# Optimization experiments

Hardware: AMD Instinct MI355X
Metric: run time of the kernel (lower is better)

## Reference

```python
import jax, jax.numpy as jnp
import numpy as np

N, E, B, IN, H = 20000, 50000, 1024, 32, 64

def setup_inputs() -> dict:
    key = jax.random.key(0)
    ks = jax.random.split(key, 32)
    d = {}
    d["x"] = jax.random.normal(ks[0], (N, IN), jnp.float32)
    d["edge_index"] = jax.random.randint(ks[1], (2, E), 0, N)
    d["edge_attr"] = jax.random.uniform(ks[2], (E, 6), dtype=jnp.float32)
    d["batch"] = jnp.sort(jax.random.randint(ks[3], (N,), 0, B))
    d["t"] = jax.random.uniform(ks[4], (B, 1), dtype=jnp.float32)
    d["p"] = jax.random.uniform(ks[5], (B, 1), dtype=jnp.float32)
    d["num_graphs"] = B
    def lin(k, fan_in, shape):
        return jax.random.normal(k, shape, jnp.float32) * (1.0 / np.sqrt(fan_in))
    # lin0: IN -> H
    d["W0"] = lin(ks[6], IN, (IN, H)); d["b0"] = jnp.zeros((H,), jnp.float32)
    # edge MLP: 6 -> 64 -> H*H
    d["We1"] = lin(ks[7], 6, (6, 64)); d["be1"] = jnp.zeros((64,), jnp.float32)
    d["We2"] = lin(ks[8], 64, (64, H * H)); d["be2"] = jnp.zeros((H * H,), jnp.float32)
    # NNConv root weight + bias
    d["Wroot"] = lin(ks[9], H, (H, H)); d["bconv"] = jnp.zeros((H,), jnp.float32)
    # GRU (input H, hidden H), torch layout [3H, *] gate order r,z,n
    d["gru_wih"] = lin(ks[10], H, (3 * H, H)); d["gru_whh"] = lin(ks[11], H, (3 * H, H))
    d["gru_bih"] = jnp.zeros((3 * H,), jnp.float32); d["gru_bhh"] = jnp.zeros((3 * H,), jnp.float32)
    # Set2Set LSTM (input 2H, hidden H), torch layout [4H, *] gate order i,f,g,o
    d["l_wih"] = lin(ks[12], 2 * H, (4 * H, 2 * H)); d["l_whh"] = lin(ks[13], H, (4 * H, H))
    d["l_bih"] = jnp.zeros((4 * H,), jnp.float32); d["l_bhh"] = jnp.zeros((4 * H,), jnp.float32)
    # readout MLP
    d["W1"] = lin(ks[14], 2 * H + 2, (2 * H + 2, H)); d["b1"] = jnp.zeros((H,), jnp.float32)
    d["W2"] = lin(ks[15], H, (H, 64)); d["b2"] = jnp.zeros((64,), jnp.float32)
    d["W3"] = lin(ks[16], 64, (64, 1)); d["b3"] = jnp.zeros((1,), jnp.float32)
    return d


def reference(x, edge_attr, t, p, W0, b0, We1, be1, We2, be2, Wroot, bconv,
              gru_wih, gru_whh, gru_bih, gru_bhh, l_wih, l_whh, l_bih, l_bhh,
              W1, b1, W2, b2, W3, b3, edge_index, batch, num_graphs):
    n_nodes = x.shape[0]
    hdim = W0.shape[1]
    src, dst = edge_index[0], edge_index[1]

    out = jax.nn.relu(x @ W0 + b0)            # [N,H]
    h = out

    # edge MLP -> per-edge weight matrices [E,H,H] (edge_attr is loop-invariant)
    ew = (jax.nn.relu(edge_attr @ We1 + be1) @ We2 + be2).reshape(-1, hdim, hdim)

    for _ in range(4):
        # NNConv: gather source features, per-edge matmul, scatter-add to targets
        msg = jnp.einsum('eh,eho->eo', out[src], ew)                 # [E,H]
        agg = jax.ops.segment_sum(msg, dst, num_segments=n_nodes)    # [N,H]
        m = jax.nn.relu(agg + out @ Wroot + bconv)
        # GRU step (single timestep)
        gi = m @ gru_wih.T + gru_bih
        gh = h @ gru_whh.T + gru_bhh
        ir, iz, inn = jnp.split(gi, 3, axis=-1)
        hr, hz, hn = jnp.split(gh, 3, axis=-1)
        r = jax.nn.sigmoid(ir + hr)
        z = jax.nn.sigmoid(iz + hz)
        nn_ = jnp.tanh(inn + r * hn)
        h = (1.0 - z) * nn_ + z * h
        out = h

    # Set2Set pooling, 3 processing steps
    qh = jnp.zeros((num_graphs, hdim), x.dtype)
    qc = jnp.zeros((num_graphs, hdim), x.dtype)
    q_star = jnp.zeros((num_graphs, 2 * hdim), x.dtype)
    for _ in range(3):
        g = q_star @ l_wih.T + l_bih + qh @ l_whh.T + l_bhh
        gi_, gf_, gg_, go_ = jnp.split(g, 4, axis=-1)
        qc = jax.nn.sigmoid(gf_) * qc + jax.nn.sigmoid(gi_) * jnp.tanh(gg_)
        qh = jax.nn.sigmoid(go_) * jnp.tanh(qc)
        q = qh                                                        # [B,H]
        e = jnp.sum(out * q[batch], axis=-1, keepdims=True)          # [N,1]
        emax = jax.ops.segment_max(e, batch, num_segments=num_graphs)
        a = jnp.exp(e - emax[batch])
        asum = jax.ops.segment_sum(a, batch, num_segments=num_graphs)
        a = a / asum[batch]                                           # segment softmax
        r_ = jax.ops.segment_sum(a * out, batch, num_segments=num_graphs)
        q_star = jnp.concatenate([q, r_], axis=-1)

    feat = jnp.concatenate([q_star, t, p], axis=-1)                   # [B,2H+2]
    y = jax.nn.relu(feat @ W1 + b1)
    y = jax.nn.relu(y @ W2 + b2)
    y = y @ W3 + b3
    return y.reshape(-1)
```

## Files before the change

kernel.cpp:

```cpp
#include <hip/hip_runtime.h>
#include <math.h>

#define N_NODES 20000
#define N_EDGES 50000
#define NB      1024
#define IND     32
#define HDIM    64

typedef __attribute__((ext_vector_type(8))) short bf16x8;
typedef __attribute__((ext_vector_type(4))) float f32x4;

static inline size_t align_up(size_t x, size_t a) { return (x + a - 1) & ~(a - 1); }

__device__ __forceinline__ float sigmoidf_(float x) {
    return 1.0f / (1.0f + __expf(-x));
}
__device__ __forceinline__ float tanhf_(float x) {
    float xc = fminf(fmaxf(x, -15.0f), 15.0f);
    float e = __expf(2.0f * xc);
    return (e - 1.0f) / (e + 1.0f);
}
__device__ __forceinline__ unsigned pk2(float p0, float p1) {
    unsigned u0 = __float_as_uint(p0) + 0x8000u;
    unsigned u1 = __float_as_uint(p1) + 0x8000u;
    return __builtin_amdgcn_perm(u1, u0, 0x07060302u);
}
__device__ __forceinline__ unsigned bf1(float v) {
    return (__float_as_uint(v) + 0x8000u) >> 16;
}

__global__ void k_prep(const float* __restrict__ We2, const float* __restrict__ be2,
                       short* __restrict__ We2b,
                       const float* __restrict__ Wroot, const float* __restrict__ gwhh,
                       const float* __restrict__ gwih,
                       short* __restrict__ WB1h, short* __restrict__ WB1l,
                       short* __restrict__ WB2h, short* __restrict__ WB2l,
                       const float* __restrict__ lwih, const float* __restrict__ lwhh,
                       float* __restrict__ lwihT, float* __restrict__ lwhhT,
                       const int* __restrict__ batch, int* __restrict__ offs,
                       const float* __restrict__ x, const float* __restrict__ W0,
                       const float* __restrict__ b0, float* __restrict__ hbuf,
                       const float* __restrict__ ea, const float* __restrict__ We1,
                       const float* __restrict__ be1, float* __restrict__ re,
                       const int* __restrict__ ei, int* __restrict__ deg) {
    int bid = blockIdx.x, tid = threadIdx.x;
    if (bid < 1040) {
        int idx = bid * 256 + tid;
        int s = idx >> 12;
        int col = idx & 4095;
        int k = col >> 6, o = col & 63;
        float val = (s < 64) ? We2[k * 4096 + s * 64 + o] : be2[k * 64 + o];
        int dst = s * 4096 + (((o >> 4) * 128 + (k >> 5) * 64 + ((k >> 3) & 3) * 16 + (o & 15)) << 3) + (k & 7);
        We2b[dst] = (short)bf1(val);
    } else if (bid < 1152) {
        int idx = (bid - 1040) * 256 + tid;
        if (idx < 28672) {
            bool b1 = idx < 16384;
            int li = b1 ? idx : idx - 16384;
            int j = li & 7, lane = (li >> 3) & 63, c = (li >> 9) & 1, otile = li >> 10;
            int k = c * 32 + (lane >> 4) * 8 + j;
            int o = otile * 16 + (lane & 15);
            float val;
            if (b1) val = (o < 64) ? Wroot[k * 64 + o] : gwhh[(o - 64) * 64 + k];
            else    val = gwih[o * 64 + k];
            unsigned hs = bf1(val);
            float lo = val - __uint_as_float(hs << 16);
            unsigned ls = bf1(lo);
            if (b1) { WB1h[li] = (short)hs; WB1l[li] = (short)ls; }
            else    { WB2h[li] = (short)hs; WB2l[li] = (short)ls; }
        }
    } else if (bid < 1280) {
        int idx = (bid - 1152) * 256 + tid;
        int i = idx >> 8, j = idx & 255;
        lwihT[idx] = lwih[j * 128 + i];
    } else if (bid < 1344) {
        int idx = (bid - 1280) * 256 + tid;
        int i = idx >> 8, j = idx & 255;
        lwhhT[idx] = lwhh[j * 64 + i];
    } else if (bid < 1349) {
        int i = (bid - 1344) * 256 + tid;
        if (i <= NB) {
            int lo = 0, hi = N_NODES;
            while (lo < hi) { int mid = (lo + hi) >> 1; if (batch[mid] < i) lo = mid + 1; else hi = mid; }
            offs[i] = lo;
        }
    } else if (bid < 6349) {
        int w = tid >> 6, j = tid & 63;
        int n = (bid - 1349) * 4 + w;
        float acc = b0[j];
        const float* xr = x + n * IND;
#pragma unroll
        for (int i = 0; i < IND; ++i) acc = fmaf(xr[i], W0[i * 64 + j], acc);
        hbuf[n * 64 + j] = fmaxf(acc, 0.0f);
    } else if (bid < 18849) {
        int w = tid >> 6, j = tid & 63;
        int e = (bid - 6349) * 4 + w;
        if (e < N_EDGES) {
            float acc = be1[j];
            const float* er = ea + e * 6;
#pragma unroll
            for (int i = 0; i < 6; ++i) acc = fmaf(er[i], We1[i * 64 + j], acc);
            re[e * 64 + j] = fmaxf(acc, 0.0f);
        }
    } else {
        int e = (bid - 18849) * 256 + tid;
        if (e < N_EDGES) atomicAdd(&deg[ei[N_EDGES + e]], 1);
    }
}

__global__ void k_scan(const int* __restrict__ deg, int* __restrict__ rowptr, int* __restrict__ cursor) {
    __shared__ int s_w[16];
    int t = threadIdx.x;
    int base = t * 20;
    int v[20]; int s = 0;
#pragma unroll
    for (int i = 0; i < 20; ++i) {
        int idx = base + i;
        v[i] = (idx < N_NODES) ? deg[idx] : 0;
        s += v[i];
    }
    int lane = t & 63, w = t >> 6;
    int inc = s;
#pragma unroll
    for (int off = 1; off < 64; off <<= 1) {
        int o = __shfl_up(inc, off);
        if (lane >= off) inc += o;
    }
    if (lane == 63) s_w[w] = inc;
    __syncthreads();
    if (w == 0 && lane < 16) {
        int x = s_w[lane];
        int xs = x;
#pragma unroll
        for (int off = 1; off < 16; off <<= 1) {
            int o = __shfl_up(xs, off);
            if (lane >= off) xs += o;
        }
        s_w[lane] = xs - x;
    }
    __syncthreads();
    int run = s_w[w] + (inc - s);
#pragma unroll
    for (int i = 0; i < 20; ++i) {
        int idx = base + i;
        if (idx < N_NODES) { rowptr[idx] = run; cursor[idx] = run; }
        else if (idx == N_NODES) rowptr[idx] = run;
        run += v[i];
    }
}

__global__ void k_fill(const int* __restrict__ ei, int* __restrict__ cursor, int* __restrict__ perm) {
    int e = blockIdx.x * 256 + threadIdx.x;
    if (e < N_EDGES) {
        int pos = atomicAdd(&cursor[ei[N_EDGES + e]], 1);
        perm[pos] = e;
    }
}

#define MSG_STEP_COMPUTE(BB0, BB1, PP)                                                              \
    _Pragma("unroll")                                                                               \
    for (int m = 0; m < 4; ++m) {                                                                   \
        f32x4 tt = __builtin_amdgcn_mfma_f32_16x16x32_bf16(BB0.v, a_re[m][0].v, zero4, 0, 0, 0);    \
        tt = __builtin_amdgcn_mfma_f32_16x16x32_bf16(BB1.v, a_re[m][1].v, tt, 0, 0, 0);             \
        macc[m][0] = fmaf(vsc[PP][m], tt[0], macc[m][0]);                                           \
        macc[m][1] = fmaf(vsc[PP][m], tt[1], macc[m][1]);                                           \
        macc[m][2] = fmaf(vsc[PP][m], tt[2], macc[m][2]);                                           \
        macc[m][3] = fmaf(vsc[PP][m], tt[3], macc[m][3]);                                           \
    }

__launch_bounds__(256, 4)
__global__ void k_msg_mfma(const float* __restrict__ hbuf, const float* __restrict__ reb,
                           const short* __restrict__ We2b, const int* __restrict__ ei,
                           float* __restrict__ msg) {
    __shared__ union {
        float v[64][64];
        float out[64][68];
    } s_u;
    int tid = threadIdx.x;
    int eb = blockIdx.x * 64;
    int lane = tid & 63;
    int w = tid >> 6;
    int l15 = lane & 15, lhi = lane >> 4;

    {
        int se = tid >> 2;
        int sh = tid & 3;
        int ge = eb + se;
        const float* rowp = (ge < N_EDGES) ? (hbuf + (size_t)ei[ge] * 64) : (const float*)0;
#pragma unroll
        for (int rr4 = 0; rr4 < 4; ++rr4) {
            int hb = rr4 * 16 + sh * 4;
            float4 vv = rowp ? *(const float4*)(rowp + hb) : make_float4(0.f, 0.f, 0.f, 0.f);
            s_u.v[hb + 0][se] = vv.x; s_u.v[hb + 1][se] = vv.y;
            s_u.v[hb + 2][se] = vv.z; s_u.v[hb + 3][se] = vv.w;
        }
    }

    union U { int4 i4; bf16x8 v; };
    U a_re[4][2];
#pragma unroll
    for (int m = 0; m < 4; ++m) {
        int ge = eb + m * 16 + l15;
        if (ge < N_EDGES) {
            const float* rp = reb + (size_t)ge * 64 + lhi * 8;
            float4 x0 = *(const float4*)(rp);
            float4 x1 = *(const float4*)(rp + 4);
            float4 y0 = *(const float4*)(rp + 32);
            float4 y1 = *(const float4*)(rp + 36);
            a_re[m][0].i4 = make_int4(pk2(x0.x, x0.y), pk2(x0.z, x0.w), pk2(x1.x, x1.y), pk2(x1.z, x1.w));
            a_re[m][1].i4 = make_int4(pk2(y0.x, y0.y), pk2(y0.z, y0.w), pk2(y1.x, y1.y), pk2(y1.z, y1.w));
        } else {
            a_re[m][0].i4 = make_int4(0, 0, 0, 0);
            a_re[m][1].i4 = make_int4(0, 0, 0, 0);
        }
    }

    const int4* bp0 = (const int4*)We2b + (w * 128 + lane);
    const int4* bp1 = bp0 + 64;
    int4 Sc0[4], Sc1[4];
#pragma unroll
    for (int j = 0; j < 4; ++j) {
        Sc0[j] = bp0[j * 512];
        Sc1[j] = bp1[j * 512];
    }

    __syncthreads();

    const f32x4 zero4 = {0.f, 0.f, 0.f, 0.f};
    f32x4 macc[4];
#pragma unroll
    for (int m = 0; m < 4; ++m) macc[m] = zero4;

    float vsc[2][4];
#pragma unroll
    for (int m = 0; m < 4; ++m) vsc[0][m] = s_u.v[0][m * 16 + l15];

    for (int g = 0; g < 16; ++g) {
#pragma unroll
        for (int j = 0; j < 4; ++j) {
            const int p = j & 1, q = p ^ 1;
            int s = g * 4 + j;
            int snext = (s < 63) ? (s + 1) : 63;
#pragma unroll
            for (int m = 0; m < 4; ++m) vsc[q][m] = s_u.v[snext][m * 16 + l15];
            U bb0, bb1; bb0.i4 = Sc0[j]; bb1.i4 = Sc1[j];
            MSG_STEP_COMPUTE(bb0, bb1, p)
            int sload = (s + 4 <= 64) ? (s + 4) : 64;
            Sc0[j] = bp0[sload * 512];
            Sc1[j] = bp1[sload * 512];
        }
    }

    {
        U bb0, bb1; bb0.i4 = Sc0[0]; bb1.i4 = Sc1[0];
#pragma unroll
        for (int m = 0; m < 4; ++m) {
            int e = m * 16 + l15;
            U a0, a1;
            a0.i4 = make_int4(
                pk2(s_u.v[lhi * 8 + 0][e], s_u.v[lhi * 8 + 1][e]),
                pk2(s_u.v[lhi * 8 + 2][e], s_u.v[lhi * 8 + 3][e]),
                pk2(s_u.v[lhi * 8 + 4][e], s_u.v[lhi * 8 + 5][e]),
                pk2(s_u.v[lhi * 8 + 6][e], s_u.v[lhi * 8 + 7][e]));
            a1.i4 = make_int4(
                pk2(s_u.v[32 + lhi * 8 + 0][e], s_u.v[32 + lhi * 8 + 1][e]),
                pk2(s_u.v[32 + lhi * 8 + 2][e], s_u.v[32 + lhi * 8 + 3][e]),
                pk2(s_u.v[32 + lhi * 8 + 4][e], s_u.v[32 + lhi * 8 + 5][e]),
                pk2(s_u.v[32 + lhi * 8 + 6][e], s_u.v[32 + lhi * 8 + 7][e]));
            macc[m] = __builtin_amdgcn_mfma_f32_16x16x32_bf16(bb0.v, a0.v, macc[m], 0, 0, 0);
            macc[m] = __builtin_amdgcn_mfma_f32_16x16x32_bf16(bb1.v, a1.v, macc[m], 0, 0, 0);
        }
    }

    __syncthreads();
#pragma unroll
    for (int m = 0; m < 4; ++m) {
        *(float4*)&s_u.out[m * 16 + l15][w * 16 + lhi * 4] =
            make_float4(macc[m][0], macc[m][1], macc[m][2], macc[m][3]);
    }
    __syncthreads();
    {
        int er = tid >> 2, qc = tid & 3;
        int ge = eb + er;
        if (ge < N_EDGES) {
#pragma unroll
            for (int i = 0; i < 4; ++i)
                *(float4*)&msg[(size_t)ge * 64 + qc * 16 + i * 4] =
                    *(const float4*)&s_u.out[er][qc * 16 + i * 4];
        }
    }
}

__launch_bounds__(256, 4)
__global__ void k_node_update(float* __restrict__ hbuf, const float* __restrict__ msg,
                              const int* __restrict__ rowptr, const int* __restrict__ perm,
                              const short* __restrict__ WB1h, const short* __restrict__ WB1l,
                              const short* __restrict__ WB2h, const short* __restrict__ WB2l,
                              const float* __restrict__ bconv, const float* __restrict__ bih,
                              const float* __restrict__ bhh) {
    __shared__ short s_hh[32][72];
    __shared__ short s_hl[32][72];
    __shared__ short s_mh[32][72];
    __shared__ short s_ml[32][72];
    __shared__ float s_agg[32][68];
    int tid = threadIdx.x;
    int nbase = blockIdx.x * 32;
    int lane = tid & 63, w = tid >> 6;
    int l15 = lane & 15, lhi = lane >> 4;

    {
        int nt = tid >> 3, q = tid & 7;
        int n = nbase + nt;
#pragma unroll
        for (int c4 = 0; c4 < 2; ++c4) {
            int col = q * 8 + c4 * 4;
            float4 v = *(const float4*)&hbuf[(size_t)n * 64 + col];
            unsigned h01 = pk2(v.x, v.y), h23 = pk2(v.z, v.w);
            float f0 = __uint_as_float(h01 << 16);
            float f1 = __uint_as_float(h01 & 0xffff0000u);
            float f2 = __uint_as_float(h23 << 16);
            float f3 = __uint_as_float(h23 & 0xffff0000u);
            unsigned l01 = pk2(v.x - f0, v.y - f1), l23 = pk2(v.z - f2, v.w - f3);
            *(unsigned*)&s_hh[nt][col]     = h01;
            *(unsigned*)&s_hh[nt][col + 2] = h23;
            *(unsigned*)&s_hl[nt][col]     = l01;
            *(unsigned*)&s_hl[nt][col + 2] = l23;
        }
        float4 aggv[2];
#pragma unroll
        for (int c4 = 0; c4 < 2; ++c4)
            aggv[c4] = *(const float4*)&bconv[q * 8 + c4 * 4];
        int rs = rowptr[n], rend = rowptr[n + 1];
        for (int qq = rs; qq < rend; ++qq) {
            const float* mrow = msg + (size_t)perm[qq] * 64 + q * 8;
#pragma unroll
            for (int c4 = 0; c4 < 2; ++c4) {
                float4 mv = *(const float4*)&mrow[c4 * 4];
                aggv[c4].x += mv.x; aggv[c4].y += mv.y;
                aggv[c4].z += mv.z; aggv[c4].w += mv.w;
            }
        }
#pragma unroll
        for (int c4 = 0; c4 < 2; ++c4)
            *(float4*)&s_agg[nt][q * 8 + c4 * 4] = aggv[c4];
    }
    __syncthreads();

    union U { int4 i4; bf16x8 v; };
    U ah[2][2], al[2][2];
#pragma unroll
    for (int m = 0; m < 2; ++m)
#pragma unroll
        for (int c = 0; c < 2; ++c) {
            ah[m][c].i4 = *(const int4*)&s_hh[m * 16 + l15][c * 32 + lhi * 8];
            al[m][c].i4 = *(const int4*)&s_hl[m * 16 + l15][c * 32 + lhi * 8];
        }

    const int4* B1h = (const int4*)WB1h;
    const int4* B1l = (const int4*)WB1l;
    const int4* B2h = (const int4*)WB2h;
    const int4* B2l = (const int4*)WB2l;

    f32x4 C0[2], G[3][2], I[3][2];

    {
        int ot = w;
        U bh0, bh1, bl0, bl1;
        bh0.i4 = B1h[(ot * 2 + 0) * 64 + lane];
        bh1.i4 = B1h[(ot * 2 + 1) * 64 + lane];
        bl0.i4 = B1l[(ot * 2 + 0) * 64 + lane];
        bl1.i4 = B1l[(ot * 2 + 1) * 64 + lane];
#pragma unroll
        for (int m = 0; m < 2; ++m) {
            f32x4 c;
#pragma unroll
            for (int r = 0; r < 4; ++r) c[r] = s_agg[m * 16 + lhi * 4 + r][w * 16 + l15];
            c = __builtin_amdgcn_mfma_f32_16x16x32_bf16(ah[m][0].v, bh0.v, c, 0, 0, 0);
            c = __builtin_amdgcn_mfma_f32_16x16x32_bf16(ah[m][1].v, bh1.v, c, 0, 0, 0);
            c = __builtin_amdgcn_mfma_f32_16x16x32_bf16(al[m][0].v, bh0.v, c, 0, 0, 0);
            c = __builtin_amdgcn_mfma_f32_16x16x32_bf16(al[m][1].v, bh1.v, c, 0, 0, 0);
            c = __builtin_amdgcn_mfma_f32_16x16x32_bf16(ah[m][0].v, bl0.v, c, 0, 0, 0);
            c = __builtin_amdgcn_mfma_f32_16x16x32_bf16(ah[m][1].v, bl1.v, c, 0, 0, 0);
            C0[m] = c;
        }
    }
#pragma unroll
    for (int m = 0; m < 2; ++m)
#pragma unroll
        for (int r = 0; r < 4; ++r) {
            float mv = fmaxf(C0[m][r], 0.0f);
            int row = m * 16 + lhi * 4 + r, col = w * 16 + l15;
            unsigned hs = bf1(mv);
            float lof = mv - __uint_as_float(hs << 16);
            s_mh[row][col] = (short)hs;
            s_ml[row][col] = (short)bf1(lof);
        }
#pragma unroll
    for (int p = 1; p < 4; ++p) {
        int ot = p * 4 + w;
        U bh0, bh1, bl0, bl1;
        bh0.i4 = B1h[(ot * 2 + 0) * 64 + lane];
        bh1.i4 = B1h[(ot * 2 + 1) * 64 + lane];
        bl0.i4 = B1l[(ot * 2 + 0) * 64 + lane];
        bl1.i4 = B1l[(ot * 2 + 1) * 64 + lane];
        float bv = bhh[(p - 1) * 64 + w * 16 + l15];
#pragma unroll
        for (int m = 0; m < 2; ++m) {
            f32x4 c = {bv, bv, bv, bv};
            c = __builtin_amdgcn_mfma_f32_16x16x32_bf16(ah[m][0].v, bh0.v, c, 0, 0, 0);
            c = __builtin_amdgcn_mfma_f32_16x16x32_bf16(ah[m][1].v, bh1.v, c, 0, 0, 0);
            c = __builtin_amdgcn_mfma_f32_16x16x32_bf16(al[m][0].v, bh0.v, c, 0, 0, 0);
            c = __builtin_amdgcn_mfma_f32_16x16x32_bf16(al[m][1].v, bh1.v, c, 0, 0, 0);
            c = __builtin_amdgcn_mfma_f32_16x16x32_bf16(ah[m][0].v, bl0.v, c, 0, 0, 0);
            c = __builtin_amdgcn_mfma_f32_16x16x32_bf16(ah[m][1].v, bl1.v, c, 0, 0, 0);
            G[p - 1][m] = c;
        }
    }
    __syncthreads();
    U mh[2][2], ml[2][2];
#pragma unroll
    for (int m = 0; m < 2; ++m)
#pragma unroll
        for (int c = 0; c < 2; ++c) {
            mh[m][c].i4 = *(const int4*)&s_mh[m * 16 + l15][c * 32 + lhi * 8];
            ml[m][c].i4 = *(const int4*)&s_ml[m * 16 + l15][c * 32 + lhi * 8];
        }
#pragma unroll
    for (int p = 0; p < 3; ++p) {
        int ot = p * 4 + w;
        U bh0, bh1, bl0, bl1;
        bh0.i4 = B2h[(ot * 2 + 0) * 64 + lane];
        bh1.i4 = B2h[(ot * 2 + 1) * 64 + lane];
        bl0.i4 = B2l[(ot * 2 + 0) * 64 + lane];
        bl1.i4 = B2l[(ot * 2 + 1) * 64 + lane];
        float bv = bih[p * 64 + w * 16 + l15];
#pragma unroll
        for (int m = 0; m < 2; ++m) {
            f32x4 c = {bv, bv, bv, bv};
            c = __builtin_amdgcn_mfma_f32_16x16x32_bf16(mh[m][0].v, bh0.v, c, 0, 0, 0);
            c = __builtin_amdgcn_mfma_f32_16x16x32_bf16(mh[m][1].v, bh1.v, c, 0, 0, 0);
            c = __builtin_amdgcn_mfma_f32_16x16x32_bf16(ml[m][0].v, bh0.v, c, 0, 0, 0);
            c = __builtin_amdgcn_mfma_f32_16x16x32_bf16(ml[m][1].v, bh1.v, c, 0, 0, 0);
            c = __builtin_amdgcn_mfma_f32_16x16x32_bf16(mh[m][0].v, bl0.v, c, 0, 0, 0);
            c = __builtin_amdgcn_mfma_f32_16x16x32_bf16(mh[m][1].v, bl1.v, c, 0, 0, 0);
            I[p][m] = c;
        }
    }
#pragma unroll
    for (int m = 0; m < 2; ++m)
#pragma unroll
        for (int r = 0; r < 4; ++r) {
            int row = m * 16 + lhi * 4 + r;
            int n = nbase + row;
            int col = w * 16 + l15;
            float hold = __uint_as_float(((unsigned)(unsigned short)s_hh[row][col]) << 16)
                       + __uint_as_float(((unsigned)(unsigned short)s_hl[row][col]) << 16);
            float rg = sigmoidf_(I[0][m][r] + G[0][m][r]);
            float z  = sigmoidf_(I[1][m][r] + G[1][m][r]);
            float nn = tanhf_(I[2][m][r] + rg * G[2][m][r]);
            hbuf[(size_t)n * 64 + col] = (1.0f - z) * nn + z * hold;
        }
}

__launch_bounds__(256)
__global__ void k_set2set(const float* __restrict__ hbuf, const int* __restrict__ offs,
                          const float* __restrict__ t, const float* __restrict__ p,
                          const float* __restrict__ lwihT, const float* __restrict__ lwhhT,
                          const float* __restrict__ l_bih, const float* __restrict__ l_bhh,
                          const float* __restrict__ W1, const float* __restrict__ b1,
                          const float* __restrict__ W2, const float* __restrict__ b2,
                          const float* __restrict__ W3, const float* __restrict__ b3,
                          float* __restrict__ y) {
    __shared__ float s_qs[192];
    __shared__ float s_g[256];
    __shared__ float s_racc[4][64];
    __shared__ float s_m[4], s_l[4];
    __shared__ float s_y[64];
    int b = blockIdx.x;
    int tid = threadIdx.x;
    int w = tid >> 6, lane = tid & 63;
    int s = offs[b], e = offs[b + 1];
    float bi = l_bih[tid] + l_bhh[tid];
    float qc = 0.f;

    if (tid < 192) s_qs[tid] = 0.f;
    __syncthreads();

    for (int iter = 0; iter < 3; ++iter) {
        float g = bi;
#pragma unroll 8
        for (int i = 0; i < 128; ++i) g = fmaf(s_qs[i], lwihT[i * 256 + tid], g);
#pragma unroll 8
        for (int i = 0; i < 64; ++i)  g = fmaf(s_qs[128 + i], lwhhT[i * 256 + tid], g);
        s_g[tid] = g;
        __syncthreads();
        if (w == 0) {
            float ci = sigmoidf_(s_g[lane]);
            float cf = sigmoidf_(s_g[64 + lane]);
            float cg = tanhf_(s_g[128 + lane]);
            float co = sigmoidf_(s_g[192 + lane]);
            qc = cf * qc + ci * cg;
            float qh = co * tanhf_(qc);
            s_qs[lane] = qh;
            s_qs[128 + lane] = qh;
        }
        __syncthreads();
        float qv = s_qs[128 + lane];
        float mx = -1e30f, l = 0.0f, racc = 0.0f;
        for (int n = s + w; n < e; n += 4) {
            float xv = hbuf[(size_t)n * 64 + lane];
            float prod = xv * qv;
#pragma unroll
            for (int off = 32; off > 0; off >>= 1) prod += __shfl_xor(prod, off);
            float mnew = fmaxf(mx, prod);
            float scale = __expf(mx - mnew);
            float wgt = __expf(prod - mnew);
            l = l * scale + wgt;
            racc = racc * scale + wgt * xv;
            mx = mnew;
        }
        s_racc[w][lane] = racc;
        if (lane == 0) { s_m[w] = mx; s_l[w] = l; }
        __syncthreads();
        if (w == 0) {
            float M = fmaxf(fmaxf(s_m[0], s_m[1]), fmaxf(s_m[2], s_m[3]));
            float L = 0.f, R = 0.f;
#pragma unroll
            for (int ww = 0; ww < 4; ++ww) {
                float sc = __expf(s_m[ww] - M);
                L += s_l[ww] * sc;
                R = fmaf(s_racc[ww][lane], sc, R);
            }
            s_qs[64 + lane] = (e > s) ? (R / L) : 0.0f;
        }
        __syncthreads();
    }
    if (w == 0) {
        float acc = b1[lane];
#pragma unroll 8
        for (int i = 0; i < 128; ++i) acc = fmaf(s_qs[i], W1[i * 64 + lane], acc);
        acc = fmaf(t[b], W1[128 * 64 + lane], acc);
        acc = fmaf(p[b], W1[129 * 64 + lane], acc);
        acc = fmaxf(acc, 0.0f);
        s_y[lane] = acc;
        float acc2 = b2[lane];
#pragma unroll 8
        for (int i = 0; i < 64; ++i) acc2 = fmaf(s_y[i], W2[i * 64 + lane], acc2);
        acc2 = fmaxf(acc2, 0.0f);
        float part = acc2 * W3[lane];
#pragma unroll
        for (int off = 32; off > 0; off >>= 1) part += __shfl_xor(part, off);
        if (lane == 0) y[b] = part + b3[0];
    }
}

extern "C" void kernel_launch(void* const* d_in, const int* in_sizes, int n_in,
                              void* d_out, int out_size, void* d_ws, size_t ws_size,
                              hipStream_t stream) {
    const float* x     = (const float*)d_in[0];
    const int*   ei    = (const int*)  d_in[1];
    const float* ea    = (const float*)d_in[2];
    const int*   batch = (const int*)  d_in[3];
    const float* t     = (const float*)d_in[4];
    const float* p     = (const float*)d_in[5];
    const float* W0    = (const float*)d_in[7];
    const float* b0    = (const float*)d_in[8];
    const float* We1   = (const float*)d_in[9];
    const float* be1   = (const float*)d_in[10];
    const float* We2   = (const float*)d_in[11];
    const float* be2   = (const float*)d_in[12];
    const float* Wroot = (const float*)d_in[13];
    const float* bconv = (const float*)d_in[14];
    const float* gwih  = (const float*)d_in[15];
    const float* gwhh  = (const float*)d_in[16];
    const float* gbih  = (const float*)d_in[17];
    const float* gbhh  = (const float*)d_in[18];
    const float* lwih  = (const float*)d_in[19];
    const float* lwhh  = (const float*)d_in[20];
    const float* lbih  = (const float*)d_in[21];
    const float* lbhh  = (const float*)d_in[22];
    const float* W1    = (const float*)d_in[23];
    const float* b1    = (const float*)d_in[24];
    const float* W2    = (const float*)d_in[25];
    const float* b2    = (const float*)d_in[26];
    const float* W3    = (const float*)d_in[27];
    const float* b3    = (const float*)d_in[28];
    float* y = (float*)d_out;

    char* ws = (char*)d_ws;
    size_t off = 0;
    auto alloc = [&](size_t nbytes) {
        void* ptr = (void*)(ws + off);
        off += align_up(nbytes, 256);
        return ptr;
    };
    float* hbuf   = (float*)alloc((size_t)N_NODES * 64 * 4);
    float* reb    = (float*)alloc((size_t)N_EDGES * 64 * 4);
    float* msg    = (float*)alloc((size_t)N_EDGES * 64 * 4);
    short* We2b   = (short*)alloc((size_t)65 * 4096 * 2);
    short* WB1h   = (short*)alloc(16384 * 2);
    short* WB1l   = (short*)alloc(16384 * 2);
    short* WB2h   = (short*)alloc(12288 * 2);
    short* WB2l   = (short*)alloc(12288 * 2);
    float* lwihT  = (float*)alloc(32768 * 4);
    float* lwhhT  = (float*)alloc(16384 * 4);
    int*   offs   = (int*)  alloc((NB + 1) * 4);
    int*   deg    = (int*)  alloc(N_NODES * 4);
    int*   rowptr = (int*)  alloc((N_NODES + 1) * 4);
    int*   cursor = (int*)  alloc(N_NODES * 4);
    int*   perm   = (int*)  alloc(N_EDGES * 4);

    hipMemsetAsync(deg, 0, (size_t)N_NODES * 4, stream);
    k_prep<<<19045, 256, 0, stream>>>(We2, be2, We2b, Wroot, gwhh, gwih,
                                      WB1h, WB1l, WB2h, WB2l,
                                      lwih, lwhh, lwihT, lwhhT, batch, offs,
                                      x, W0, b0, hbuf, ea, We1, be1, reb,
                                      ei, deg);
    k_scan<<<1, 1024, 0, stream>>>(deg, rowptr, cursor);
    k_fill<<<(N_EDGES + 255) / 256, 256, 0, stream>>>(ei, cursor, perm);

    for (int it = 0; it < 4; ++it) {
        k_msg_mfma<<<(N_EDGES + 63) / 64, 256, 0, stream>>>(hbuf, reb, We2b, ei, msg);
        k_node_update<<<N_NODES / 32, 256, 0, stream>>>(hbuf, msg, rowptr, perm,
                                                        WB1h, WB1l, WB2h, WB2l,
                                                        bconv, gbih, gbhh);
    }

    k_set2set<<<NB, 256, 0, stream>>>(hbuf, offs, t, p, lwihT, lwhhT, lbih, lbhh,
                                      W1, b1, W2, b2, W3, b3, y);
}
```

Baseline: 412.7 us.

## Stage We2 slices through LDS ring via global_load_lds and widen block to 256 edges

The message kernel now handles 256 edges per block, with each wave owning 64 edges and all four output tiles, rather than 64 edges split across waves by output tile. The bf16 We2 weight slices are streamed into a 4-slot LDS ring using direct global-to-LDS loads three steps ahead, synchronised with waitcnt and barriers, and then read from LDS into registers. This cuts redundant global/L2 weight traffic by a factor of four per edge and overlaps the weight fetch with MFMA work. In exchange it uses much more LDS and registers (launch bounds drop to 1 block per SM hint), gives fewer blocks (196) for 256 CUs, and adds a barrier per step.

Result: slower. 442.0 us (+7.1%).

```diff
diff --git a/kernel.cpp b/kernel.cpp
--- a/kernel.cpp
+++ b/kernel.cpp
@@ -157,42 +157,75 @@
     }
 }
 
-#define MSG_STEP_COMPUTE(BB0, BB1, PP)                                                              \
-    _Pragma("unroll")                                                                               \
-    for (int m = 0; m < 4; ++m) {                                                                   \
-        f32x4 tt = __builtin_amdgcn_mfma_f32_16x16x32_bf16(BB0.v, a_re[m][0].v, zero4, 0, 0, 0);    \
-        tt = __builtin_amdgcn_mfma_f32_16x16x32_bf16(BB1.v, a_re[m][1].v, tt, 0, 0, 0);             \
-        macc[m][0] = fmaf(vsc[PP][m], tt[0], macc[m][0]);                                           \
-        macc[m][1] = fmaf(vsc[PP][m], tt[1], macc[m][1]);                                           \
-        macc[m][2] = fmaf(vsc[PP][m], tt[2], macc[m][2]);                                           \
-        macc[m][3] = fmaf(vsc[PP][m], tt[3], macc[m][3]);                                           \
-    }
-
-__launch_bounds__(256, 4)
+#define MSG_STEP(CF, NF, CV, NV, S, DO_STAGE, VMC)                                                  \
+    {                                                                                               \
+        asm volatile("s_waitcnt vmcnt(" #VMC ")" ::: "memory");                                     \
+        __builtin_amdgcn_s_barrier();                                                               \
+        int slot_r = ((S) + 1) & 3;                                                                 \
+        _Pragma("unroll")                                                                           \
+        for (int ot = 0; ot < 4; ++ot) {                                                            \
+            NF[ot][0].i4 = s_ring[slot_r][ot * 128 + lane];                                         \
+            NF[ot][1].i4 = s_ring[slot_r][ot * 128 + 64 + lane];                                    \
+        }                                                                                           \
+        int svn = ((S) + 1 < 64) ? ((S) + 1) : 63;                                                  \
+        _Pragma("unroll")                                                                           \
+        for (int m = 0; m < 4; ++m) NV[m] = s_u.v[svn][ebase + m * 16 + l15];                       \
+        if (DO_STAGE) {                                                                             \
+            int slot_w = ((S) + 3) & 3;                                                             \
+            const int4* srcq = gW + (size_t)((S) + 3) * 512 + w * 128;                              \
+            __builtin_amdgcn_global_load_lds(                                                       \
+                (const __attribute__((address_space(1))) int4*)(srcq + lane),                       \
+                (__attribute__((address_space(3))) int4*)&s_ring[slot_w][w * 128], 16, 0, 0);       \
+            __builtin_amdgcn_global_load_lds(                                                       \
+                (const __attribute__((address_space(1))) int4*)(srcq + 64 + lane),                  \
+                (__attribute__((address_space(3))) int4*)&s_ring[slot_w][w * 128 + 64], 16, 0, 0);  \
+        }                                                                                           \
+        _Pragma("unroll")                                                                           \
+        for (int ot = 0; ot < 4; ++ot) {                                                            \
+            _Pragma("unroll")                                                                       \
+            for (int m = 0; m < 4; ++m) {                                                           \
+                f32x4 tt = __builtin_amdgcn_mfma_f32_16x16x32_bf16(CF[ot][0].v, a_re[m][0].v, zero4, 0, 0, 0); \
+                tt = __builtin_amdgcn_mfma_f32_16x16x32_bf16(CF[ot][1].v, a_re[m][1].v, tt, 0, 0, 0);          \
+                macc[ot][m][0] = fmaf(CV[m], tt[0], macc[ot][m][0]);                                \
+                macc[ot][m][1] = fmaf(CV[m], tt[1], macc[ot][m][1]);                                \
+                macc[ot][m][2] = fmaf(CV[m], tt[2], macc[ot][m][2]);                                \
+                macc[ot][m][3] = fmaf(CV[m], tt[3], macc[ot][m][3]);                                \
+            }                                                                                       \
+        }                                                                                           \
+        asm volatile("s_waitcnt lgkmcnt(0)" ::: "memory");                                          \
+        __builtin_amdgcn_sched_barrier(0);                                                          \
+    }
+
+__launch_bounds__(256, 1)
 __global__ void k_msg_mfma(const float* __restrict__ hbuf, const float* __restrict__ reb,
                            const short* __restrict__ We2b, const int* __restrict__ ei,
                            float* __restrict__ msg) {
     __shared__ union {
-        float v[64][64];
-        float out[64][68];
+        float v[64][256];
+        float out[256][68];
     } s_u;
+    __shared__ int4 s_ring[4][512];
     int tid = threadIdx.x;
-    int eb = blockIdx.x * 64;
+    int eb = blockIdx.x * 256;
     int lane = tid & 63;
     int w = tid >> 6;
     int l15 = lane & 15, lhi = lane >> 4;
+    int ebase = w * 64;
 
     {
-        int se = tid >> 2;
-        int sh = tid & 3;
-        int ge = eb + se;
-        const float* rowp = (ge < N_EDGES) ? (hbuf + (size_t)ei[ge] * 64) : (const float*)0;
-#pragma unroll
-        for (int rr4 = 0; rr4 < 4; ++rr4) {
-            int hb = rr4 * 16 + sh * 4;
-            float4 vv = rowp ? *(const float4*)(rowp + hb) : make_float4(0.f, 0.f, 0.f, 0.f);
-            s_u.v[hb + 0][se] = vv.x; s_u.v[hb + 1][se] = vv.y;
-            s_u.v[hb + 2][se] = vv.z; s_u.v[hb + 3][se] = vv.w;
+        int se = tid >> 2, sh = tid & 3;
+#pragma unroll
+        for (int pass = 0; pass < 4; ++pass) {
+            int le = pass * 64 + se;
+            int ge = eb + le;
+            const float* rowp = (ge < N_EDGES) ? (hbuf + (size_t)ei[ge] * 64) : (const float*)0;
+#pragma unroll
+            for (int rr4 = 0; rr4 < 4; ++rr4) {
+                int hb = rr4 * 16 + sh * 4;
+                float4 vv = rowp ? *(const float4*)(rowp + hb) : make_float4(0.f, 0.f, 0.f, 0.f);
+                s_u.v[hb + 0][le] = vv.x; s_u.v[hb + 1][le] = vv.y;
+                s_u.v[hb + 2][le] = vv.z; s_u.v[hb + 3][le] = vv.w;
+            }
         }
     }
 
@@ -200,7 +233,7 @@
     U a_re[4][2];
 #pragma unroll
     for (int m = 0; m < 4; ++m) {
-        int ge = eb + m * 16 + l15;
+        int ge = eb + ebase + m * 16 + l15;
         if (ge < N_EDGES) {
             const float* rp = reb + (size_t)ge * 64 + lhi * 8;
             float4 x0 = *(const float4*)(rp);
@@ -215,78 +248,92 @@
         }
     }
 
-    const int4* bp0 = (const int4*)We2b + (w * 128 + lane);
-    const int4* bp1 = bp0 + 64;
-    int4 Sc0[4], Sc1[4];
-#pragma unroll
-    for (int j = 0; j < 4; ++j) {
-        Sc0[j] = bp0[j * 512];
-        Sc1[j] = bp1[j * 512];
-    }
-
-    __syncthreads();
+    __syncthreads();
+
+    const int4* gW = (const int4*)We2b;
+
+#pragma unroll
+    for (int r = 0; r < 3; ++r) {
+        const int4* srcq = gW + (size_t)r * 512 + w * 128;
+        __builtin_amdgcn_global_load_lds(
+            (const __attribute__((address_space(1))) int4*)(srcq + lane),
+            (__attribute__((address_space(3))) int4*)&s_ring[r][w * 128], 16, 0, 0);
+        __builtin_amdgcn_global_load_lds(
+            (const __attribute__((address_space(1))) int4*)(srcq + 64 + lane),
+            (__attribute__((address_space(3))) int4*)&s_ring[r][w * 128 + 64], 16, 0, 0);
+    }
 
     const f32x4 zero4 = {0.f, 0.f, 0.f, 0.f};
-    f32x4 macc[4];
-#pragma unroll
-    for (int m = 0; m < 4; ++m) macc[m] = zero4;
-
-    float vsc[2][4];
-#pragma unroll
-    for (int m = 0; m < 4; ++m) vsc[0][m] = s_u.v[0][m * 16 + l15];
-
-    for (int g = 0; g < 16; ++g) {
-#pragma unroll
-        for (int j = 0; j < 4; ++j) {
-            const int p = j & 1, q = p ^ 1;
-            int s = g * 4 + j;
-            int snext = (s < 63) ? (s + 1) : 63;
-#pragma unroll
-            for (int m = 0; m < 4; ++m) vsc[q][m] = s_u.v[snext][m * 16 + l15];
-            U bb0, bb1; bb0.i4 = Sc0[j]; bb1.i4 = Sc1[j];
-            MSG_STEP_COMPUTE(bb0, bb1, p)
-            int sload = (s + 4 <= 64) ? (s + 4) : 64;
-            Sc0[j] = bp0[sload * 512];
-            Sc1[j] = bp1[sload * 512];
-        }
-    }
-
-    {
-        U bb0, bb1; bb0.i4 = Sc0[0]; bb1.i4 = Sc1[0];
-#pragma unroll
-        for (int m = 0; m < 4; ++m) {
-            int e = m * 16 + l15;
-            U a0, a1;
-            a0.i4 = make_int4(
-                pk2(s_u.v[lhi * 8 + 0][e], s_u.v[lhi * 8 + 1][e]),
-                pk2(s_u.v[lhi * 8 + 2][e], s_u.v[lhi * 8 + 3][e]),
-                pk2(s_u.v[lhi * 8 + 4][e], s_u.v[lhi * 8 + 5][e]),
-                pk2(s_u.v[lhi * 8 + 6][e], s_u.v[lhi * 8 + 7][e]));
-            a1.i4 = make_int4(
-                pk2(s_u.v[32 + lhi * 8 + 0][e], s_u.v[32 + lhi * 8 + 1][e]),
-                pk2(s_u.v[32 + lhi * 8 + 2][e], s_u.v[32 + lhi * 8 + 3][e]),
-                pk2(s_u.v[32 + lhi * 8 + 4][e], s_u.v[32 + lhi * 8 + 5][e]),
-                pk2(s_u.v[32 + lhi * 8 + 6][e], s_u.v[32 + lhi * 8 + 7][e]));
-            macc[m] = __builtin_amdgcn_mfma_f32_16x16x32_bf16(bb0.v, a0.v, macc[m], 0, 0, 0);
-            macc[m] = __builtin_amdgcn_mfma_f32_16x16x32_bf16(bb1.v, a1.v, macc[m], 0, 0, 0);
-        }
-    }
-
-    __syncthreads();
+    f32x4 macc[4][4];
+#pragma unroll
+    for (int ot = 0; ot < 4; ++ot)
+#pragma unroll
+        for (int m = 0; m < 4; ++m) macc[ot][m] = zero4;
+
+    U F0[4][2], F1[4][2];
+    float vs0[4], vs1[4];
+
+    asm volatile("s_waitcnt vmcnt(4)" ::: "memory");
+    __builtin_amdgcn_s_barrier();
+#pragma unroll
+    for (int ot = 0; ot < 4; ++ot) {
+        F0[ot][0].i4 = s_ring[0][ot * 128 + lane];
+        F0[ot][1].i4 = s_ring[0][ot * 128 + 64 + lane];
+    }
+#pragma unroll
+    for (int m = 0; m < 4; ++m) vs0[m] = s_u.v[0][ebase + m * 16 + l15];
+    asm volatile("s_waitcnt lgkmcnt(0)" ::: "memory");
+    __builtin_amdgcn_sched_barrier(0);
+
+    for (int g = 0; g < 31; ++g) {
+        int s0 = g * 2;
+        MSG_STEP(F0, F1, vs0, vs1, s0, 1, 2)
+        MSG_STEP(F1, F0, vs1, vs0, s0 + 1, 1, 2)
+    }
+    MSG_STEP(F0, F1, vs0, vs1, 62, 0, 2)
+    MSG_STEP(F1, F0, vs1, vs0, 63, 0, 0)
+
 #pragma unroll
     for (int m = 0; m < 4; ++m) {
-        *(float4*)&s_u.out[m * 16 + l15][w * 16 + lhi * 4] =
-            make_float4(macc[m][0], macc[m][1], macc[m][2], macc[m][3]);
-    }
+        int e = ebase + m * 16 + l15;
+        U a0, a1;
+        a0.i4 = make_int4(
+            pk2(s_u.v[lhi * 8 + 0][e], s_u.v[lhi * 8 + 1][e]),
+            pk2(s_u.v[lhi * 8 + 2][e], s_u.v[lhi * 8 + 3][e]),
+            pk2(s_u.v[lhi * 8 + 4][e], s_u.v[lhi * 8 + 5][e]),
+            pk2(s_u.v[lhi * 8 + 6][e], s_u.v[lhi * 8 + 7][e]));
+        a1.i4 = make_int4(
+            pk2(s_u.v[32 + lhi * 8 + 0][e], s_u.v[32 + lhi * 8 + 1][e]),
+            pk2(s_u.v[32 + lhi * 8 + 2][e], s_u.v[32 + lhi * 8 + 3][e]),
+            pk2(s_u.v[32 + lhi * 8 + 4][e], s_u.v[32 + lhi * 8 + 5][e]),
+            pk2(s_u.v[32 + lhi * 8 + 6][e], s_u.v[32 + lhi * 8 + 7][e]));
+#pragma unroll
+        for (int ot = 0; ot < 4; ++ot) {
+            macc[ot][m] = __builtin_amdgcn_mfma_f32_16x16x32_bf16(F0[ot][0].v, a0.v, macc[ot][m], 0, 0, 0);
+            macc[ot][m] = __builtin_amdgcn_mfma_f32_16x16x32_bf16(F0[ot][1].v, a1.v, macc[ot][m], 0, 0, 0);
+        }
+    }
+
+    __syncthreads();
+#pragma unroll
+    for (int ot = 0; ot < 4; ++ot)
+#pragma unroll
+        for (int m = 0; m < 4; ++m)
+            *(float4*)&s_u.out[ebase + m * 16 + l15][ot * 16 + lhi * 4] =
+                make_float4(macc[ot][m][0], macc[ot][m][1], macc[ot][m][2], macc[ot][m][3]);
     __syncthreads();
     {
         int er = tid >> 2, qc = tid & 3;
-        int ge = eb + er;
-        if (ge < N_EDGES) {
-#pragma unroll
-            for (int i = 0; i < 4; ++i)
-                *(float4*)&msg[(size_t)ge * 64 + qc * 16 + i * 4] =
-                    *(const float4*)&s_u.out[er][qc * 16 + i * 4];
+#pragma unroll
+        for (int pass = 0; pass < 4; ++pass) {
+            int row = pass * 64 + er;
+            int ge = eb + row;
+            if (ge < N_EDGES) {
+#pragma unroll
+                for (int i = 0; i < 4; ++i)
+                    *(float4*)&msg[(size_t)ge * 64 + qc * 16 + i * 4] =
+                        *(const float4*)&s_u.out[row][qc * 16 + i * 4];
+            }
         }
     }
 }
@@ -620,7 +667,7 @@
     k_fill<<<(N_EDGES + 255) / 256, 256, 0, stream>>>(ei, cursor, perm);
 
     for (int it = 0; it < 4; ++it) {
-        k_msg_mfma<<<(N_EDGES + 63) / 64, 256, 0, stream>>>(hbuf, reb, We2b, ei, msg);
+        k_msg_mfma<<<(N_EDGES + 255) / 256, 256, 0, stream>>>(hbuf, reb, We2b, ei, msg);
         k_node_update<<<N_NODES / 32, 256, 0, stream>>>(hbuf, msg, rowptr, perm,
                                                         WB1h, WB1l, WB2h, WB2l,
                                                         bconv, gbih, gbhh);
```

## Stage We2 through an LDS ring with async loads and widen message tiles

Applied to the files above, without the earlier changes.

The message kernel now handles 256 edges per block with 512 threads, up from 64 edges with 256 threads. The bf16 We2 weight slices are streamed into an 8-slot shared-memory ring using global_load_lds, prefetched 6 steps ahead, instead of each wave loading them from global memory into registers. Each weight slice fetched from global memory is therefore reused across 4x more edges, and the loads overlap with MFMA compute. The cost is a block barrier on every step, much larger LDS use (64KB for node features plus 64KB for the ring), and more accumulator registers, all of which lower occupancy.

Result: slower. 480.3 us (+16.4%).

```diff
diff --git a/kernel.cpp b/kernel.cpp
--- a/kernel.cpp
+++ b/kernel.cpp
@@ -157,39 +157,60 @@
     }
 }
 
-#define MSG_STEP_COMPUTE(BB0, BB1, PP)                                                              \
-    _Pragma("unroll")                                                                               \
-    for (int m = 0; m < 4; ++m) {                                                                   \
-        f32x4 tt = __builtin_amdgcn_mfma_f32_16x16x32_bf16(BB0.v, a_re[m][0].v, zero4, 0, 0, 0);    \
-        tt = __builtin_amdgcn_mfma_f32_16x16x32_bf16(BB1.v, a_re[m][1].v, tt, 0, 0, 0);             \
-        macc[m][0] = fmaf(vsc[PP][m], tt[0], macc[m][0]);                                           \
-        macc[m][1] = fmaf(vsc[PP][m], tt[1], macc[m][1]);                                           \
-        macc[m][2] = fmaf(vsc[PP][m], tt[2], macc[m][2]);                                           \
-        macc[m][3] = fmaf(vsc[PP][m], tt[3], macc[m][3]);                                           \
-    }
-
-__launch_bounds__(256, 4)
+#define MSG_STEP(CF, NF, PC, PN, S, DO_STAGE, VMC)                                                  \
+    {                                                                                               \
+        asm volatile("s_waitcnt vmcnt(" #VMC ")" ::: "memory");                                     \
+        __builtin_amdgcn_s_barrier();                                                               \
+        int slot_r = ((S) + 1) & 7;                                                                 \
+        NF[0].i4 = s_ring[slot_r][wo * 128 + lane];                                                 \
+        NF[1].i4 = s_ring[slot_r][wo * 128 + 64 + lane];                                            \
+        int svn = ((S) + 1 < 64) ? ((S) + 1) : 63;                                                  \
+        _Pragma("unroll")                                                                           \
+        for (int m = 0; m < 8; ++m) vsc[PN][m] = s_u.v[svn][ebase + m * 16 + l15];                  \
+        if (DO_STAGE) {                                                                             \
+            const int4* srcq = gW + (size_t)((S) + 6) * 512 + w * 64;                               \
+            __builtin_amdgcn_global_load_lds(                                                       \
+                (const __attribute__((address_space(1))) int4*)(srcq + lane),                       \
+                (__attribute__((address_space(3))) int4*)&s_ring[((S) + 6) & 7][w * 64], 16, 0, 0); \
+        }                                                                                           \
+        _Pragma("unroll")                                                                           \
+        for (int m = 0; m < 8; ++m) {                                                               \
+            f32x4 tt = __builtin_amdgcn_mfma_f32_16x16x32_bf16(CF[0].v, a_re[m][0].v, zero4, 0, 0, 0); \
+            tt = __builtin_amdgcn_mfma_f32_16x16x32_bf16(CF[1].v, a_re[m][1].v, tt, 0, 0, 0);       \
+            macc[m][0] = fmaf(vsc[PC][m], tt[0], macc[m][0]);                                       \
+            macc[m][1] = fmaf(vsc[PC][m], tt[1], macc[m][1]);                                       \
+            macc[m][2] = fmaf(vsc[PC][m], tt[2], macc[m][2]);                                       \
+            macc[m][3] = fmaf(vsc[PC][m], tt[3], macc[m][3]);                                       \
+        }                                                                                           \
+        asm volatile("s_waitcnt lgkmcnt(0)" ::: "memory");                                          \
+        __builtin_amdgcn_sched_barrier(0);                                                          \
+    }
+
+__launch_bounds__(512, 2)
 __global__ void k_msg_mfma(const float* __restrict__ hbuf, const float* __restrict__ reb,
                            const short* __restrict__ We2b, const int* __restrict__ ei,
                            float* __restrict__ msg) {
     __shared__ union {
-        float v[64][64];
-        float out[64][68];
+        float v[64][256];
+        float out[256][68];
     } s_u;
+    __shared__ int4 s_ring[8][512];
     int tid = threadIdx.x;
-    int eb = blockIdx.x * 64;
+    int eb = blockIdx.x * 256;
     int lane = tid & 63;
     int w = tid >> 6;
+    int wo = w & 3;
+    int we = w >> 2;
     int l15 = lane & 15, lhi = lane >> 4;
+    int ebase = we * 128;
 
     {
-        int se = tid >> 2;
-        int sh = tid & 3;
+        int se = tid >> 1, sh = tid & 1;
         int ge = eb + se;
         const float* rowp = (ge < N_EDGES) ? (hbuf + (size_t)ei[ge] * 64) : (const float*)0;
 #pragma unroll
-        for (int rr4 = 0; rr4 < 4; ++rr4) {
-            int hb = rr4 * 16 + sh * 4;
+        for (int rr4 = 0; rr4 < 8; ++rr4) {
+            int hb = sh * 32 + rr4 * 4;
             float4 vv = rowp ? *(const float4*)(rowp + hb) : make_float4(0.f, 0.f, 0.f, 0.f);
             s_u.v[hb + 0][se] = vv.x; s_u.v[hb + 1][se] = vv.y;
             s_u.v[hb + 2][se] = vv.z; s_u.v[hb + 3][se] = vv.w;
@@ -197,10 +218,10 @@
     }
 
     union U { int4 i4; bf16x8 v; };
-    U a_re[4][2];
-#pragma unroll
-    for (int m = 0; m < 4; ++m) {
-        int ge = eb + m * 16 + l15;
+    U a_re[8][2];
+#pragma unroll
+    for (int m = 0; m < 8; ++m) {
+        int ge = eb + ebase + m * 16 + l15;
         if (ge < N_EDGES) {
             const float* rp = reb + (size_t)ge * 64 + lhi * 8;
             float4 x0 = *(const float4*)(rp);
@@ -215,78 +236,79 @@
         }
     }
 
-    const int4* bp0 = (const int4*)We2b + (w * 128 + lane);
-    const int4* bp1 = bp0 + 64;
-    int4 Sc0[4], Sc1[4];
-#pragma unroll
-    for (int j = 0; j < 4; ++j) {
-        Sc0[j] = bp0[j * 512];
-        Sc1[j] = bp1[j * 512];
-    }
-
-    __syncthreads();
+    __syncthreads();
+
+    const int4* gW = (const int4*)We2b;
+
+#pragma unroll
+    for (int r = 0; r < 6; ++r) {
+        const int4* srcq = gW + (size_t)r * 512 + w * 64;
+        __builtin_amdgcn_global_load_lds(
+            (const __attribute__((address_space(1))) int4*)(srcq + lane),
+            (__attribute__((address_space(3))) int4*)&s_ring[r][w * 64], 16, 0, 0);
+    }
 
     const f32x4 zero4 = {0.f, 0.f, 0.f, 0.f};
-    f32x4 macc[4];
-#pragma unroll
-    for (int m = 0; m < 4; ++m) macc[m] = zero4;
-
-    float vsc[2][4];
-#pragma unroll
-    for (int m = 0; m < 4; ++m) vsc[0][m] = s_u.v[0][m * 16 + l15];
-
-    for (int g = 0; g < 16; ++g) {
-#pragma unroll
-        for (int j = 0; j < 4; ++j) {
-            const int p = j & 1, q = p ^ 1;
-            int s = g * 4 + j;
-            int snext = (s < 63) ? (s + 1) : 63;
-#pragma unroll
-            for (int m = 0; m < 4; ++m) vsc[q][m] = s_u.v[snext][m * 16 + l15];
-            U bb0, bb1; bb0.i4 = Sc0[j]; bb1.i4 = Sc1[j];
-            MSG_STEP_COMPUTE(bb0, bb1, p)
-            int sload = (s + 4 <= 64) ? (s + 4) : 64;
-            Sc0[j] = bp0[sload * 512];
-            Sc1[j] = bp1[sload * 512];
-        }
-    }
-
+    f32x4 macc[8];
+#pragma unroll
+    for (int m = 0; m < 8; ++m) macc[m] = zero4;
+
+    U F0[2], F1[2];
+    float vsc[2][8];
+
+    asm volatile("s_waitcnt vmcnt(5)" ::: "memory");
+    __builtin_amdgcn_s_barrier();
+    F0[0].i4 = s_ring[0][wo * 128 + lane];
+    F0[1].i4 = s_ring[0][wo * 128 + 64 + lane];
+#pragma unroll
+    for (int m = 0; m < 8; ++m) vsc[0][m] = s_u.v[0][ebase + m * 16 + l15];
+    asm volatile("s_waitcnt lgkmcnt(0)" ::: "memory");
+    __builtin_amdgcn_sched_barrier(0);
+
+    for (int g = 0; g < 29; ++g) {
+        int s0 = g * 2;
+        MSG_STEP(F0, F1, 0, 1, s0, 1, 4)
+        MSG_STEP(F1, F0, 1, 0, s0 + 1, 1, 4)
+    }
+    MSG_STEP(F0, F1, 0, 1, 58, 1, 4)
+    MSG_STEP(F1, F0, 1, 0, 59, 0, 4)
+    MSG_STEP(F0, F1, 0, 1, 60, 0, 3)
+    MSG_STEP(F1, F0, 1, 0, 61, 0, 2)
+    MSG_STEP(F0, F1, 0, 1, 62, 0, 1)
+    MSG_STEP(F1, F0, 1, 0, 63, 0, 0)
+
+#pragma unroll
+    for (int m = 0; m < 8; ++m) {
+        int e = ebase + m * 16 + l15;
+        U a0, a1;
+        a0.i4 = make_int4(
+            pk2(s_u.v[lhi * 8 + 0][e], s_u.v[lhi * 8 + 1][e]),
+            pk2(s_u.v[lhi * 8 + 2][e], s_u.v[lhi * 8 + 3][e]),
+            pk2(s_u.v[lhi * 8 + 4][e], s_u.v[lhi * 8 + 5][e]),
+            pk2(s_u.v[lhi * 8 + 6][e], s_u.v[lhi * 8 + 7][e]));
+        a1.i4 = make_int4(
+            pk2(s_u.v[32 + lhi * 8 + 0][e], s_u.v[32 + lhi * 8 + 1][e]),
+            pk2(s_u.v[32 + lhi * 8 + 2][e], s_u.v[32 + lhi * 8 + 3][e]),
+            pk2(s_u.v[32 + lhi * 8 + 4][e], s_u.v[32 + lhi * 8 + 5][e]),
+            pk2(s_u.v[32 + lhi * 8 + 6][e], s_u.v[32 + lhi * 8 + 7][e]));
+        macc[m] = __builtin_amdgcn_mfma_f32_16x16x32_bf16(F0[0].v, a0.v, macc[m], 0, 0, 0);
+        macc[m] = __builtin_amdgcn_mfma_f32_16x16x32_bf16(F0[1].v, a1.v, macc[m], 0, 0, 0);
+    }
+
+    __syncthreads();
+#pragma unroll
+    for (int m = 0; m < 8; ++m)
+        *(float4*)&s_u.out[ebase + m * 16 + l15][wo * 16 + lhi * 4] =
+            make_float4(macc[m][0], macc[m][1], macc[m][2], macc[m][3]);
+    __syncthreads();
     {
-        U bb0, bb1; bb0.i4 = Sc0[0]; bb1.i4 = Sc1[0];
-#pragma unroll
-        for (int m = 0; m < 4; ++m) {
-            int e = m * 16 + l15;
-            U a0, a1;
-            a0.i4 = make_int4(
-                pk2(s_u.v[lhi * 8 + 0][e], s_u.v[lhi * 8 + 1][e]),
-                pk2(s_u.v[lhi * 8 + 2][e], s_u.v[lhi * 8 + 3][e]),
-                pk2(s_u.v[lhi * 8 + 4][e], s_u.v[lhi * 8 + 5][e]),
-                pk2(s_u.v[lhi * 8 + 6][e], s_u.v[lhi * 8 + 7][e]));
-            a1.i4 = make_int4(
-                pk2(s_u.v[32 + lhi * 8 + 0][e], s_u.v[32 + lhi * 8 + 1][e]),
-                pk2(s_u.v[32 + lhi * 8 + 2][e], s_u.v[32 + lhi * 8 + 3][e]),
-                pk2(s_u.v[32 + lhi * 8 + 4][e], s_u.v[32 + lhi * 8 + 5][e]),
-                pk2(s_u.v[32 + lhi * 8 + 6][e], s_u.v[32 + lhi * 8 + 7][e]));
-            macc[m] = __builtin_amdgcn_mfma_f32_16x16x32_bf16(bb0.v, a0.v, macc[m], 0, 0, 0);
-            macc[m] = __builtin_amdgcn_mfma_f32_16x16x32_bf16(bb1.v, a1.v, macc[m], 0, 0, 0);
-        }
-    }
-
-    __syncthreads();
-#pragma unroll
-    for (int m = 0; m < 4; ++m) {
-        *(float4*)&s_u.out[m * 16 + l15][w * 16 + lhi * 4] =
-            make_float4(macc[m][0], macc[m][1], macc[m][2], macc[m][3]);
-    }
-    __syncthreads();
-    {
-        int er = tid >> 2, qc = tid & 3;
+        int er = tid >> 1, qc = tid & 1;
         int ge = eb + er;
         if (ge < N_EDGES) {
 #pragma unroll
-            for (int i = 0; i < 4; ++i)
-                *(float4*)&msg[(size_t)ge * 64 + qc * 16 + i * 4] =
-                    *(const float4*)&s_u.out[er][qc * 16 + i * 4];
+            for (int i = 0; i < 8; ++i)
+                *(float4*)&msg[(size_t)ge * 64 + qc * 32 + i * 4] =
+                    *(const float4*)&s_u.out[er][qc * 32 + i * 4];
         }
     }
 }
@@ -620,7 +642,7 @@
     k_fill<<<(N_EDGES + 255) / 256, 256, 0, stream>>>(ei, cursor, perm);
 
     for (int it = 0; it < 4; ++it) {
-        k_msg_mfma<<<(N_EDGES + 63) / 64, 256, 0, stream>>>(hbuf, reb, We2b, ei, msg);
+        k_msg_mfma<<<(N_EDGES + 255) / 256, 512, 0, stream>>>(hbuf, reb, We2b, ei, msg);
         k_node_update<<<N_NODES / 32, 256, 0, stream>>>(hbuf, msg, rowptr, perm,
                                                         WB1h, WB1l, WB2h, WB2l,
                                                         bconv, gbih, gbhh);
```

## Process four graphs per set2set block, sharing LSTM weight loads

Applied to the files above, without the earlier changes.

The set2set kernel now handles four graphs per block, one per wavefront. Each LSTM gate weight load is reused across four graphs, and the cross-wave online-softmax merge is dropped because each wave scans its own graph's nodes serially. This cuts global weight traffic and block count by four. In exchange, each graph's attention loop runs on a single wave instead of four, which lengthens the serial node scan per graph.

After: 436.5 us. +5.8%, slower.

```diff
diff --git a/kernel.cpp b/kernel.cpp
--- a/kernel.cpp
+++ b/kernel.cpp
@@ -471,43 +471,56 @@
                           const float* __restrict__ W2, const float* __restrict__ b2,
                           const float* __restrict__ W3, const float* __restrict__ b3,
                           float* __restrict__ y) {
-    __shared__ float s_qs[192];
-    __shared__ float s_g[256];
-    __shared__ float s_racc[4][64];
-    __shared__ float s_m[4], s_l[4];
-    __shared__ float s_y[64];
-    int b = blockIdx.x;
+    __shared__ float s_qs[4][192];
+    __shared__ float s_g[4][256];
+    __shared__ float s_y[4][64];
     int tid = threadIdx.x;
     int w = tid >> 6, lane = tid & 63;
-    int s = offs[b], e = offs[b + 1];
+    int gb = blockIdx.x * 4;
+    int s = offs[gb + w], e = offs[gb + w + 1];
     float bi = l_bih[tid] + l_bhh[tid];
     float qc = 0.f;
 
-    if (tid < 192) s_qs[tid] = 0.f;
+    if (tid < 192) {
+        s_qs[0][tid] = 0.f; s_qs[1][tid] = 0.f;
+        s_qs[2][tid] = 0.f; s_qs[3][tid] = 0.f;
+    }
     __syncthreads();
 
     for (int iter = 0; iter < 3; ++iter) {
-        float g = bi;
+        float g0 = bi, g1 = bi, g2 = bi, g3 = bi;
 #pragma unroll 8
-        for (int i = 0; i < 128; ++i) g = fmaf(s_qs[i], lwihT[i * 256 + tid], g);
+        for (int i = 0; i < 128; ++i) {
+            float wv = lwihT[i * 256 + tid];
+            g0 = fmaf(s_qs[0][i], wv, g0);
+            g1 = fmaf(s_qs[1][i], wv, g1);
+            g2 = fmaf(s_qs[2][i], wv, g2);
+            g3 = fmaf(s_qs[3][i], wv, g3);
+        }
 #pragma unroll 8
-        for (int i = 0; i < 64; ++i)  g = fmaf(s_qs[128 + i], lwhhT[i * 256 + tid], g);
-        s_g[tid] = g;
+        for (int i = 0; i < 64; ++i) {
+            float wv = lwhhT[i * 256 + tid];
+            g0 = fmaf(s_qs[0][128 + i], wv, g0);
+            g1 = fmaf(s_qs[1][128 + i], wv, g1);
+            g2 = fmaf(s_qs[2][128 + i], wv, g2);
+            g3 = fmaf(s_qs[3][128 + i], wv, g3);
+        }
+        s_g[0][tid] = g0; s_g[1][tid] = g1; s_g[2][tid] = g2; s_g[3][tid] = g3;
         __syncthreads();
-        if (w == 0) {
-            float ci = sigmoidf_(s_g[lane]);
-            float cf = sigmoidf_(s_g[64 + lane]);
-            float cg = tanhf_(s_g[128 + lane]);
-            float co = sigmoidf_(s_g[192 + lane]);
+
+        {
+            float ci = sigmoidf_(s_g[w][lane]);
+            float cf = sigmoidf_(s_g[w][64 + lane]);
+            float cg = tanhf_(s_g[w][128 + lane]);
+            float co = sigmoidf_(s_g[w][192 + lane]);
             qc = cf * qc + ci * cg;
             float qh = co * tanhf_(qc);
-            s_qs[lane] = qh;
-            s_qs[128 + lane] = qh;
-        }
-        __syncthreads();
-        float qv = s_qs[128 + lane];
+            s_qs[w][lane] = qh;
+            s_qs[w][128 + lane] = qh;
+        }
+        float qv = s_qs[w][128 + lane];
         float mx = -1e30f, l = 0.0f, racc = 0.0f;
-        for (int n = s + w; n < e; n += 4) {
+        for (int n = s; n < e; ++n) {
             float xv = hbuf[(size_t)n * 64 + lane];
             float prod = xv * qv;
 #pragma unroll
@@ -519,38 +532,26 @@
             racc = racc * scale + wgt * xv;
             mx = mnew;
         }
-        s_racc[w][lane] = racc;
-        if (lane == 0) { s_m[w] = mx; s_l[w] = l; }
+        s_qs[w][64 + lane] = (e > s) ? (racc / l) : 0.0f;
         __syncthreads();
-        if (w == 0) {
-            float M = fmaxf(fmaxf(s_m[0], s_m[1]), fmaxf(s_m[2], s_m[3]));
-            float L = 0.f, R = 0.f;
-#pragma unroll
-            for (int ww = 0; ww < 4; ++ww) {
-                float sc = __expf(s_m[ww] - M);
-                L += s_l[ww] * sc;
-                R = fmaf(s_racc[ww][lane], sc, R);
-            }
-            s_qs[64 + lane] = (e > s) ? (R / L) : 0.0f;
-        }
-        __syncthreads();
-    }
-    if (w == 0) {
+    }
+
+    {
         float acc = b1[lane];
 #pragma unroll 8
-        for (int i = 0; i < 128; ++i) acc = fmaf(s_qs[i], W1[i * 64 + lane], acc);
-        acc = fmaf(t[b], W1[128 * 64 + lane], acc);
-        acc = fmaf(p[b], W1[129 * 64 + lane], acc);
+        for (int i = 0; i < 128; ++i) acc = fmaf(s_qs[w][i], W1[i * 64 + lane], acc);
+        acc = fmaf(t[gb + w], W1[128 * 64 + lane], acc);
+        acc = fmaf(p[gb + w], W1[129 * 64 + lane], acc);
         acc = fmaxf(acc, 0.0f);
-        s_y[lane] = acc;
+        s_y[w][lane] = acc;
         float acc2 = b2[lane];
 #pragma unroll 8
-        for (int i = 0; i < 64; ++i) acc2 = fmaf(s_y[i], W2[i * 64 + lane], acc2);
+        for (int i = 0; i < 64; ++i) acc2 = fmaf(s_y[w][i], W2[i * 64 + lane], acc2);
         acc2 = fmaxf(acc2, 0.0f);
         float part = acc2 * W3[lane];
 #pragma unroll
         for (int off = 32; off > 0; off >>= 1) part += __shfl_xor(part, off);
-        if (lane == 0) y[b] = part + b3[0];
+        if (lane == 0) y[gb + w] = part + b3[0];
     }
 }
 
@@ -626,6 +627,6 @@
                                                         bconv, gbih, gbhh);
     }
 
-    k_set2set<<<NB, 256, 0, stream>>>(hbuf, offs, t, p, lwihT, lwhhT, lbih, lbhh,
-                                      W1, b1, W2, b2, W3, b3, y);
-}
+    k_set2set<<<NB / 4, 256, 0, stream>>>(hbuf, offs, t, p, lwihT, lwhhT, lbih, lbhh,
+                                          W1, b1, W2, b2, W3, b3, y);
+}
```
